# Performance work log

Measured on AMD Instinct MI355X. Metric: run time of the kernel, lower is better.

Reference implementation:

```python
import jax, jax.numpy as jnp
import numpy as np

B, C, H, W = 4, 64, 64, 64
INTER = 16  # in_c // k


def setup_inputs() -> dict:
    key = jax.random.key(0)
    ks = jax.random.split(key, 12)
    sC = 1.0 / np.sqrt(C)
    sI = 1.0 / np.sqrt(INTER)
    return {
        "x":   jax.random.normal(ks[0], (B, C, H, W), dtype=jnp.float32),
        "Wq":  jax.random.normal(ks[1], (INTER, C), dtype=jnp.float32) * sC,
        "bq":  jax.random.normal(ks[2], (INTER,), dtype=jnp.float32) * 0.1,
        "Wk":  jax.random.normal(ks[3], (INTER, C), dtype=jnp.float32) * sC,
        "bk":  jax.random.normal(ks[4], (INTER,), dtype=jnp.float32) * 0.1,
        "wcq": jax.random.normal(ks[5], (INTER,), dtype=jnp.float32) * sI,
        "wck": jax.random.normal(ks[6], (INTER,), dtype=jnp.float32) * sI,
        "Wv":  jax.random.normal(ks[7], (C, C), dtype=jnp.float32) * sC,
        "bv":  jax.random.normal(ks[8], (C,), dtype=jnp.float32) * 0.1,
        "Wg":  jax.random.normal(ks[9], (C, C), dtype=jnp.float32) * sC,
        "bg":  jax.random.normal(ks[10], (C,), dtype=jnp.float32) * 0.1,
    }


def reference(x, Wq, bq, Wk, bk, wcq, wck, Wv, bv, Wg, bg):
    b_, c_, h_, w_ = x.shape
    n = h_ * w_
    xf = x.reshape(b_, c_, n)  # (B, C, N)
    # 1x1 conv projections (per-pixel linear maps)
    q = jnp.einsum('oc,bcn->bon', Wq, xf) + bq[None, :, None]  # (B, inter, N)
    k = jnp.einsum('oc,bcn->bon', Wk, xf) + bk[None, :, None]  # (B, inter, N)
    # concat_conv (1x1, no bias) over [q_i ; k_j] decomposes into an outer sum:
    # energy[b,i,j] = wcq . q[b,:,i] + wck . k[b,:,j]
    a = jnp.einsum('o,bon->bn', wcq, q)  # (B, N)
    d = jnp.einsum('o,bon->bn', wck, k)  # (B, N)
    energy = jax.nn.elu(a[:, :, None] + d[:, None, :])  # (B, N, N)
    energy = energy / (1.5 * jnp.sum(energy, axis=1, keepdims=True))
    v = jnp.einsum('oc,bcn->bon', Wv, xf) + bv[None, :, None]  # (B, C, N)
    out = jnp.einsum('bci,bij->bcj', v, energy)  # (B, C, N)
    # gamma 1x1 conv
    out = jnp.einsum('oc,bcn->bon', Wg, out) + bg[None, :, None]
    return out.reshape(b_, c_, h_, w_)
```

## Files before the change

kernel.cpp:

```cpp
#include <hip/hip_runtime.h>
#include <math.h>

#define NB 4096

#define BARo   0
#define RELo   16
#define GHo    272
#define GCNTo  16656
#define Do     49424
#define VGo    65808
#define ASo    1114384
#define PERMo  1130768
#define BSTo   1147152
#define Po     1163536
#define PSEAo  1212688
#define PSAo   1212944
#define CPo    1213200
#define CPSEAo 1263380
#define CPSAo  1263640
#define MEMSET_BYTES 132160

__device__ __forceinline__ float gld(const float* p) {
    return __hip_atomic_load(p, __ATOMIC_RELAXED, __HIP_MEMORY_SCOPE_AGENT);
}
__device__ __forceinline__ void gst(float* p, float v) {
    __hip_atomic_store(p, v, __ATOMIC_RELAXED, __HIP_MEMORY_SCOPE_AGENT);
}
__device__ __forceinline__ void gsti(int* p, int v) {
    __hip_atomic_store(p, v, __ATOMIC_RELAXED, __HIP_MEMORY_SCOPE_AGENT);
}

__device__ __forceinline__ int bucket_of(float v) {
    int k = (int)((v + 16.0f) * 128.0f);
    k = k < 0 ? 0 : k;
    k = k > (NB - 1) ? (NB - 1) : k;
    return k;
}

__device__ __forceinline__ void gbar(int* wsi, int idx, int n) {
    __syncthreads();
    if (threadIdx.x == 0) {
        int old = __hip_atomic_fetch_add(wsi + BARo + idx, 1, __ATOMIC_RELAXED,
                                         __HIP_MEMORY_SCOPE_AGENT);
        if (old == n - 1) {
#pragma unroll
            for (int i = 0; i < 8; i++)
                __hip_atomic_store(wsi + RELo + i * 32, idx + 1, __ATOMIC_RELAXED,
                                   __HIP_MEMORY_SCOPE_AGENT);
        } else {
            const int* myrel = wsi + RELo + (blockIdx.x & 7) * 32;
            while (__hip_atomic_load(myrel, __ATOMIC_RELAXED, __HIP_MEMORY_SCOPE_AGENT) <= idx)
                __builtin_amdgcn_s_sleep(8);
        }
    }
    __syncthreads();
}

__global__ __launch_bounds__(256, 1) void k_fused(
        const float* __restrict__ x,
        const float* __restrict__ Wq, const float* __restrict__ bq,
        const float* __restrict__ Wk, const float* __restrict__ bk,
        const float* __restrict__ wcq, const float* __restrict__ wck,
        const float* __restrict__ Wv, const float* __restrict__ bv,
        const float* __restrict__ Wg, const float* __restrict__ bg,
        float* __restrict__ ws, float* __restrict__ out) {
    __shared__ float smem[13056];
    int tid = threadIdx.x;
    int bid = blockIdx.x;
    int b = bid >> 6, t6 = bid & 63;
    int* wsi = (int*)ws;
    int* gh  = wsi + GHo;

    float myA = 0.f;

    {
        float* xt  = smem;
        float* wt  = smem + 4352;
        float* wqe = smem + 8704, *wke = smem + 8768, *bvg = smem + 8832, *misc = smem + 8896;
        if (tid < 64) {
            float s1 = 0.f, s2 = 0.f, s3 = 0.f;
            for (int o = 0; o < 16; o++) { s1 += wcq[o] * Wq[o * 64 + tid]; s2 += wck[o] * Wk[o * 64 + tid]; }
            for (int m = 0; m < 64; m++) s3 += Wg[tid * 64 + m] * bv[m];
            wqe[tid] = s1; wke[tid] = s2; bvg[tid] = s3;
        } else if (tid == 64) {
            float s = 0.f; for (int o = 0; o < 16; o++) s += wcq[o] * bq[o]; misc[0] = s;
        } else if (tid == 65) {
            float s = 0.f; for (int o = 0; o < 16; o++) s += wck[o] * bk[o]; misc[1] = s;
        }
        {
            int o = tid & 63, c0 = (tid >> 6) * 16;
            float acc[16];
#pragma unroll
            for (int k = 0; k < 16; k++) acc[k] = 0.f;
            for (int m = 0; m < 64; m++) {
                float wg = Wg[o * 64 + m];
                const float4* wv4 = (const float4*)(Wv + m * 64 + c0);
                float4 a0 = wv4[0], a1 = wv4[1], a2 = wv4[2], a3 = wv4[3];
                acc[0] += wg * a0.x; acc[1] += wg * a0.y; acc[2] += wg * a0.z; acc[3] += wg * a0.w;
                acc[4] += wg * a1.x; acc[5] += wg * a1.y; acc[6] += wg * a1.z; acc[7] += wg * a1.w;
                acc[8] += wg * a2.x; acc[9] += wg * a2.y; acc[10] += wg * a2.z; acc[11] += wg * a2.w;
                acc[12] += wg * a3.x; acc[13] += wg * a3.y; acc[14] += wg * a3.z; acc[15] += wg * a3.w;
            }
#pragma unroll
            for (int k = 0; k < 16; k++) wt[(c0 + k) * 68 + o] = acc[k];
        }
        const float* xb = x + (size_t)b * 64 * 4096;
        for (int idx = tid; idx < 4096; idx += 256) {
            int c = idx >> 6, nl = idx & 63;
            xt[c * 68 + nl] = xb[(size_t)c * 4096 + t6 * 64 + nl];
        }
        __syncthreads();
        if (tid < 64) {
            float s1 = misc[0], s2 = misc[1];
            for (int c = 0; c < 64; c++) {
                float xv = xt[c * 68 + tid];
                s1 += wqe[c] * xv; s2 += wke[c] * xv;
            }
            myA = s1;
            ws[Do + b * 4096 + t6 * 64 + tid] = s2;
            atomicAdd(&gh[b * 4096 + bucket_of(s1)], 1);
        }
        {
            int o = tid & 63, nl0 = (tid >> 6) * 16;
            float acc[16];
            float bo = bvg[o];
#pragma unroll
            for (int k = 0; k < 16; k++) acc[k] = bo;
            for (int c = 0; c < 64; c++) {
                float wv = wt[c * 68 + o];
                const float* xr = &xt[c * 68 + nl0];
#pragma unroll
                for (int k = 0; k < 16; k++) acc[k] += wv * xr[k];
            }
#pragma unroll
            for (int k = 0; k < 16; k++)
                gst(&ws[VGo + ((size_t)(b * 4096) + t6 * 64 + nl0 + k) * 64 + o], acc[k]);
        }
    }
    gbar(wsi, 0, 256);

    {
        unsigned int* hist = (unsigned int*)smem;
        unsigned int* scanbuf = hist + 4096;
        const int* gh_b = gh + b * 4096;
        int* gcnt = wsi + GCNTo + b * 4096;
#pragma unroll 4
        for (int i = tid; i < NB; i += 256) hist[i] = (unsigned int)gh_b[i];
        __syncthreads();
        unsigned int s = 0u; int base = tid * 16;
        for (int k = 0; k < 16; k++) s += hist[base + k];
        scanbuf[tid] = s;
        __syncthreads();
        for (int off = 1; off < 256; off <<= 1) {
            unsigned int v = scanbuf[tid];
            unsigned int u = (tid >= off) ? scanbuf[tid - off] : 0u;
            __syncthreads();
            scanbuf[tid] = v + u;
            __syncthreads();
        }
        unsigned int run = (tid > 0) ? scanbuf[tid - 1] : 0u;
        for (int k = 0; k < 16; k++) {
            unsigned int h = hist[base + k];
            hist[base + k] = run;
            run += h;
        }
        __syncthreads();
        if (t6 == 0) {
            int* bst = wsi + BSTo;
#pragma unroll 4
            for (int i = tid; i < NB; i += 256) gsti(&bst[b * 4096 + i], (int)hist[i]);
        }
        if (tid < 64) {
            int i = t6 * 64 + tid;
            int kb = bucket_of(myA);
            int r = (int)hist[kb] + atomicAdd(&gcnt[kb], 1);
            gst(&ws[ASo + b * 4096 + r], myA);
            gsti((int*)ws + PERMo + b * 4096 + r, i);
        }
    }
    gbar(wsi, 1, 256);

    {
        int c = tid & 63, w = tid >> 6;
        int r0 = t6 * 64 + w * 16;
        const int* perm = (const int*)ws + PERMo;
        int pk[16]; float avs[16], wvs[16];
#pragma unroll
        for (int k = 0; k < 16; k++) pk[k] = perm[b * 4096 + r0 + k];
#pragma unroll
        for (int k = 0; k < 16; k++) avs[k] = ws[ASo + b * 4096 + r0 + k];
#pragma unroll
        for (int k = 0; k < 16; k++) wvs[k] = ws[VGo + ((size_t)(b * 4096) + pk[k]) * 64 + c];
        float s1 = 0.f, s2 = 0.f, s3 = 0.f, sea_w = 0.f, sa_w = 0.f;
#pragma unroll
        for (int k = 0; k < 16; k++) {
            float ea = expf(avs[k]);
            s1 += wvs[k]; s2 += wvs[k] * ea; s3 += wvs[k] * avs[k];
            sea_w += ea; sa_w += avs[k];
        }
        float* partL = smem;
        float* wsc   = smem + 768;
        partL[(w * 3 + 0) * 64 + c] = s1;
        partL[(w * 3 + 1) * 64 + c] = s2;
        partL[(w * 3 + 2) * 64 + c] = s3;
        if (c == 0) { wsc[w] = sea_w; wsc[4 + w] = sa_w; }
        __syncthreads();
        if (tid < 192) {
            int g = tid >> 6, cc = tid & 63;
            float s = partL[(0 * 3 + g) * 64 + cc] + partL[(1 * 3 + g) * 64 + cc]
                    + partL[(2 * 3 + g) * 64 + cc] + partL[(3 * 3 + g) * 64 + cc];
            gst(&ws[Po + (b * 64 + t6) * 192 + tid], s);
        } else if (tid == 192) {
            gst(&ws[PSEAo + b * 64 + t6], wsc[0] + wsc[1] + wsc[2] + wsc[3]);
            gst(&ws[PSAo  + b * 64 + t6], wsc[4] + wsc[5] + wsc[6] + wsc[7]);
        }
    }
    gbar(wsi, 2, 256);

    {
        if (tid < 192) {
            float s = 0.f;
#pragma unroll 8
            for (int ch = 0; ch < t6; ch++) s += ws[Po + b * 12288 + ch * 192 + tid];
            gst(&ws[CPo + b * 12545 + t6 * 193 + tid], s);
            if (t6 == 63) {
                s += ws[Po + b * 12288 + 63 * 192 + tid];
                gst(&ws[CPo + b * 12545 + 64 * 193 + tid], s);
            }
        } else if (tid == 192) {
            float s = 0.f;
            for (int ch = 0; ch < t6; ch++) s += ws[PSEAo + b * 64 + ch];
            gst(&ws[CPSEAo + b * 65 + t6], s);
            if (t6 == 63) { s += ws[PSEAo + b * 64 + 63]; gst(&ws[CPSEAo + b * 65 + 64], s); }
        } else if (tid == 193) {
            float s = 0.f;
            for (int ch = 0; ch < t6; ch++) s += ws[PSAo + b * 64 + ch];
            gst(&ws[CPSAo + b * 65 + t6], s);
            if (t6 == 63) { s += ws[PSAo + b * 64 + 63]; gst(&ws[CPSAo + b * 65 + 64], s); }
        }
    }
    gbar(wsi, 3, 256);

    {
        float* cpsea  = smem + 12545;
        float* cpsa   = smem + 12610;
        float* djs    = smem + 12675;
        float* edjs   = smem + 12739;
        float* invden = smem + 12803;
        int*   qarr   = (int*)(smem + 12867);
        float* bgs    = smem + 12931;
        for (int i = tid; i < 12545; i += 256) smem[i] = ws[CPo + b * 12545 + i];
        if (tid < 65)                     cpsea[tid] = ws[CPSEAo + b * 65 + tid];
        else if (tid >= 128 && tid < 193) cpsa[tid - 128] = ws[CPSAo + b * 65 + tid - 128];
        else if (tid >= 64 && tid < 128)  bgs[tid - 64] = bg[tid - 64];
        __syncthreads();
        const int* bst = (const int*)ws + BSTo;
        int j0 = t6 * 64;
        if (tid < 64) {
            int j = j0 + tid;
            float dj = ws[Do + b * 4096 + j];
            float edj = expf(dj);
            int kb = bucket_of(-dj);
            int t = bst[b * NB + kb];
            int q = (t + 32) >> 6;
            float den = 1.5f * ((cpsa[64] - cpsa[q]) + dj * (float)(4096 - 64 * q)
                                - (float)(64 * q) + edj * cpsea[q]);
            qarr[tid] = q; djs[tid] = dj; edjs[tid] = edj; invden[tid] = 1.0f / den;
        }
        __syncthreads();
        {
            int jl = tid & 63, cq = tid >> 6;
            float dj = djs[jl], edj = edjs[jl], inv = invden[jl];
            int qb = qarr[jl] * 193;
            for (int cc = cq; cc < 64; cc += 4) {
                float c1 = smem[qb + cc], c2 = smem[qb + 64 + cc], c3 = smem[qb + 128 + cc];
                float t1 = smem[12352 + cc], t3 = smem[12352 + 128 + cc];
                float num = (t3 - c3) + dj * t1 - (1.0f + dj) * c1 + edj * c2;
                out[((size_t)(b * 64 + cc)) * 4096 + j0 + jl] = num * inv + bgs[cc];
            }
        }
    }
}

extern "C" void kernel_launch(void* const* d_in, const int* in_sizes, int n_in,
                              void* d_out, int out_size, void* d_ws, size_t ws_size,
                              hipStream_t stream) {
    const float* x   = (const float*)d_in[0];
    const float* Wq  = (const float*)d_in[1];
    const float* bq  = (const float*)d_in[2];
    const float* Wk  = (const float*)d_in[3];
    const float* bk  = (const float*)d_in[4];
    const float* wcq = (const float*)d_in[5];
    const float* wck = (const float*)d_in[6];
    const float* Wv  = (const float*)d_in[7];
    const float* bv  = (const float*)d_in[8];
    const float* Wg  = (const float*)d_in[9];
    const float* bg  = (const float*)d_in[10];
    float* ws  = (float*)d_ws;
    float* out = (float*)d_out;

    hipMemsetAsync(d_ws, 0, MEMSET_BYTES, stream);
    k_fused<<<256, 256, 0, stream>>>(x, Wq, bq, Wk, bk, wcq, wck, Wv, bv, Wg, bg, ws, out);
}
```

Measured before the change: 124.5 us.

## Use hierarchical grid barrier, drop prefix stage, use wave-shuffle scan

Replaces the single-counter grid barrier with a two-level tree: leaf counters of 32 blocks feed a master counter, which cuts contention on one atomic. Removes the fourth grid barrier and the global prefix-sum stage. Each block now rebuilds the full chunk prefix sums redundantly in shared memory from the partials. The histogram scan now uses wave shuffles instead of a barrier-heavy shared-memory scan, and x tiles are loaded as float4 with a stride padded to 72. The price is that every block reads all 64 partials per column, which adds redundant global reads and register pressure from the 64-element arrays.

```diff
diff --git a/kernel.cpp b/kernel.cpp
--- a/kernel.cpp
+++ b/kernel.cpp
@@ -3,26 +3,21 @@
 
 #define NB 4096
 
-#define BARo   0
-#define RELo   16
-#define GHo    272
-#define GCNTo  16656
-#define Do     49424
-#define VGo    65808
-#define ASo    1114384
-#define PERMo  1130768
-#define BSTo   1147152
-#define Po     1163536
-#define PSEAo  1212688
-#define PSAo   1212944
-#define CPo    1213200
-#define CPSEAo 1263380
-#define CPSAo  1263640
-#define MEMSET_BYTES 132160
-
-__device__ __forceinline__ float gld(const float* p) {
-    return __hip_atomic_load(p, __ATOMIC_RELAXED, __HIP_MEMORY_SCOPE_AGENT);
-}
+#define LEAFo  0
+#define MASTo  768
+#define RELo   864
+#define GHo    1120
+#define GCNTo  17504
+#define MEMSET_BYTES 135552
+#define Do     33888
+#define VGo    50272
+#define ASo    1098848
+#define PERMo  1115232
+#define BSTo   1131616
+#define Po     1148000
+#define PSEAo  1197152
+#define PSAo   1197408
+
 __device__ __forceinline__ void gst(float* p, float v) {
     __hip_atomic_store(p, v, __ATOMIC_RELAXED, __HIP_MEMORY_SCOPE_AGENT);
 }
@@ -37,18 +32,26 @@
     return k;
 }
 
-__device__ __forceinline__ void gbar(int* wsi, int idx, int n) {
+__device__ __forceinline__ void gbar(int* wsi, int idx) {
     __syncthreads();
     if (threadIdx.x == 0) {
-        int old = __hip_atomic_fetch_add(wsi + BARo + idx, 1, __ATOMIC_RELAXED,
-                                         __HIP_MEMORY_SCOPE_AGENT);
-        if (old == n - 1) {
-#pragma unroll
-            for (int i = 0; i < 8; i++)
-                __hip_atomic_store(wsi + RELo + i * 32, idx + 1, __ATOMIC_RELAXED,
-                                   __HIP_MEMORY_SCOPE_AGENT);
-        } else {
-            const int* myrel = wsi + RELo + (blockIdx.x & 7) * 32;
+        int leaf = blockIdx.x & 7;
+        bool bcast = false;
+        int old = __hip_atomic_fetch_add(wsi + LEAFo + (idx * 8 + leaf) * 32, 1,
+                                         __ATOMIC_RELAXED, __HIP_MEMORY_SCOPE_AGENT);
+        if (old == 31) {
+            int m = __hip_atomic_fetch_add(wsi + MASTo + idx * 32, 1,
+                                           __ATOMIC_RELAXED, __HIP_MEMORY_SCOPE_AGENT);
+            if (m == 7) {
+#pragma unroll
+                for (int i = 0; i < 8; i++)
+                    __hip_atomic_store(wsi + RELo + i * 32, idx + 1,
+                                       __ATOMIC_RELAXED, __HIP_MEMORY_SCOPE_AGENT);
+                bcast = true;
+            }
+        }
+        if (!bcast) {
+            const int* myrel = wsi + RELo + leaf * 32;
             while (__hip_atomic_load(myrel, __ATOMIC_RELAXED, __HIP_MEMORY_SCOPE_AGENT) <= idx)
                 __builtin_amdgcn_s_sleep(8);
         }
@@ -75,8 +78,8 @@
 
     {
         float* xt  = smem;
-        float* wt  = smem + 4352;
-        float* wqe = smem + 8704, *wke = smem + 8768, *bvg = smem + 8832, *misc = smem + 8896;
+        float* wt  = smem + 4608;
+        float* wqe = smem + 9216, *wke = smem + 9280, *bvg = smem + 9344, *misc = smem + 9408;
         if (tid < 64) {
             float s1 = 0.f, s2 = 0.f, s3 = 0.f;
             for (int o = 0; o < 16; o++) { s1 += wcq[o] * Wq[o * 64 + tid]; s2 += wck[o] * Wk[o * 64 + tid]; }
@@ -102,18 +105,19 @@
                 acc[12] += wg * a3.x; acc[13] += wg * a3.y; acc[14] += wg * a3.z; acc[15] += wg * a3.w;
             }
 #pragma unroll
-            for (int k = 0; k < 16; k++) wt[(c0 + k) * 68 + o] = acc[k];
-        }
-        const float* xb = x + (size_t)b * 64 * 4096;
-        for (int idx = tid; idx < 4096; idx += 256) {
-            int c = idx >> 6, nl = idx & 63;
-            xt[c * 68 + nl] = xb[(size_t)c * 4096 + t6 * 64 + nl];
+            for (int k = 0; k < 16; k++) wt[(c0 + k) * 72 + o] = acc[k];
+        }
+        const float4* xb4 = (const float4*)(x + (size_t)b * 64 * 4096);
+#pragma unroll
+        for (int idx = tid; idx < 1024; idx += 256) {
+            int c = idx >> 4, nl4 = idx & 15;
+            *(float4*)&xt[c * 72 + nl4 * 4] = xb4[c * 1024 + t6 * 16 + nl4];
         }
         __syncthreads();
         if (tid < 64) {
             float s1 = misc[0], s2 = misc[1];
             for (int c = 0; c < 64; c++) {
-                float xv = xt[c * 68 + tid];
+                float xv = xt[c * 72 + tid];
                 s1 += wqe[c] * xv; s2 += wke[c] * xv;
             }
             myA = s1;
@@ -127,8 +131,8 @@
 #pragma unroll
             for (int k = 0; k < 16; k++) acc[k] = bo;
             for (int c = 0; c < 64; c++) {
-                float wv = wt[c * 68 + o];
-                const float* xr = &xt[c * 68 + nl0];
+                float wv = wt[c * 72 + o];
+                const float* xr = &xt[c * 72 + nl0];
 #pragma unroll
                 for (int k = 0; k < 16; k++) acc[k] += wv * xr[k];
             }
@@ -137,28 +141,29 @@
                 gst(&ws[VGo + ((size_t)(b * 4096) + t6 * 64 + nl0 + k) * 64 + o], acc[k]);
         }
     }
-    gbar(wsi, 0, 256);
+    gbar(wsi, 0);
 
     {
         unsigned int* hist = (unsigned int*)smem;
-        unsigned int* scanbuf = hist + 4096;
+        unsigned int* wtot = hist + 4096;
         const int* gh_b = gh + b * 4096;
         int* gcnt = wsi + GCNTo + b * 4096;
 #pragma unroll 4
         for (int i = tid; i < NB; i += 256) hist[i] = (unsigned int)gh_b[i];
         __syncthreads();
+        int lane = tid & 63, w = tid >> 6;
         unsigned int s = 0u; int base = tid * 16;
+#pragma unroll
         for (int k = 0; k < 16; k++) s += hist[base + k];
-        scanbuf[tid] = s;
-        __syncthreads();
-        for (int off = 1; off < 256; off <<= 1) {
-            unsigned int v = scanbuf[tid];
-            unsigned int u = (tid >= off) ? scanbuf[tid - off] : 0u;
-            __syncthreads();
-            scanbuf[tid] = v + u;
-            __syncthreads();
-        }
-        unsigned int run = (tid > 0) ? scanbuf[tid - 1] : 0u;
+        unsigned int inc = s;
+        for (int off = 1; off < 64; off <<= 1) {
+            unsigned int u = __shfl_up(inc, off);
+            if (lane >= off) inc += u;
+        }
+        if (lane == 63) wtot[w] = inc;
+        __syncthreads();
+        unsigned int run = inc - s;
+        for (int w2 = 0; w2 < w; w2++) run += wtot[w2];
         for (int k = 0; k < 16; k++) {
             unsigned int h = hist[base + k];
             hist[base + k] = run;
@@ -178,7 +183,7 @@
             gsti((int*)ws + PERMo + b * 4096 + r, i);
         }
     }
-    gbar(wsi, 1, 256);
+    gbar(wsi, 1);
 
     {
         int c = tid & 63, w = tid >> 6;
@@ -215,33 +220,10 @@
             gst(&ws[PSAo  + b * 64 + t6], wsc[4] + wsc[5] + wsc[6] + wsc[7]);
         }
     }
-    gbar(wsi, 2, 256);
+    gbar(wsi, 2);
 
     {
-        if (tid < 192) {
-            float s = 0.f;
-#pragma unroll 8
-            for (int ch = 0; ch < t6; ch++) s += ws[Po + b * 12288 + ch * 192 + tid];
-            gst(&ws[CPo + b * 12545 + t6 * 193 + tid], s);
-            if (t6 == 63) {
-                s += ws[Po + b * 12288 + 63 * 192 + tid];
-                gst(&ws[CPo + b * 12545 + 64 * 193 + tid], s);
-            }
-        } else if (tid == 192) {
-            float s = 0.f;
-            for (int ch = 0; ch < t6; ch++) s += ws[PSEAo + b * 64 + ch];
-            gst(&ws[CPSEAo + b * 65 + t6], s);
-            if (t6 == 63) { s += ws[PSEAo + b * 64 + 63]; gst(&ws[CPSEAo + b * 65 + 64], s); }
-        } else if (tid == 193) {
-            float s = 0.f;
-            for (int ch = 0; ch < t6; ch++) s += ws[PSAo + b * 64 + ch];
-            gst(&ws[CPSAo + b * 65 + t6], s);
-            if (t6 == 63) { s += ws[PSAo + b * 64 + 63]; gst(&ws[CPSAo + b * 65 + 64], s); }
-        }
-    }
-    gbar(wsi, 3, 256);
-
-    {
+        float* CP     = smem;
         float* cpsea  = smem + 12545;
         float* cpsa   = smem + 12610;
         float* djs    = smem + 12675;
@@ -249,10 +231,34 @@
         float* invden = smem + 12803;
         int*   qarr   = (int*)(smem + 12867);
         float* bgs    = smem + 12931;
-        for (int i = tid; i < 12545; i += 256) smem[i] = ws[CPo + b * 12545 + i];
-        if (tid < 65)                     cpsea[tid] = ws[CPSEAo + b * 65 + tid];
-        else if (tid >= 128 && tid < 193) cpsa[tid - 128] = ws[CPSAo + b * 65 + tid - 128];
-        else if (tid >= 64 && tid < 128)  bgs[tid - 64] = bg[tid - 64];
+        if (tid < 192) {
+            float v[64];
+#pragma unroll
+            for (int ch = 0; ch < 64; ch++) v[ch] = ws[Po + b * 12288 + ch * 192 + tid];
+            float r = 0.f;
+#pragma unroll
+            for (int q = 0; q < 64; q++) { CP[q * 193 + tid] = r; r += v[q]; }
+            CP[64 * 193 + tid] = r;
+        } else if (tid == 192) {
+            float v[64];
+#pragma unroll
+            for (int ch = 0; ch < 64; ch++) v[ch] = ws[PSEAo + b * 64 + ch];
+            float r = 0.f;
+#pragma unroll
+            for (int q = 0; q < 64; q++) { cpsea[q] = r; r += v[q]; }
+            cpsea[64] = r;
+        } else if (tid == 193) {
+            float v[64];
+#pragma unroll
+            for (int ch = 0; ch < 64; ch++) v[ch] = ws[PSAo + b * 64 + ch];
+            float r = 0.f;
+#pragma unroll
+            for (int q = 0; q < 64; q++) { cpsa[q] = r; r += v[q]; }
+            cpsa[64] = r;
+        } else if (tid >= 194 && tid < 258) {
+        }
+        if (tid >= 194 - 64 && tid < 194) { }
+        if (tid < 64) bgs[tid] = bg[tid];
         __syncthreads();
         const int* bst = (const int*)ws + BSTo;
         int j0 = t6 * 64;
@@ -273,8 +279,8 @@
             float dj = djs[jl], edj = edjs[jl], inv = invden[jl];
             int qb = qarr[jl] * 193;
             for (int cc = cq; cc < 64; cc += 4) {
-                float c1 = smem[qb + cc], c2 = smem[qb + 64 + cc], c3 = smem[qb + 128 + cc];
-                float t1 = smem[12352 + cc], t3 = smem[12352 + 128 + cc];
+                float c1 = CP[qb + cc], c2 = CP[qb + 64 + cc], c3 = CP[qb + 128 + cc];
+                float t1 = CP[64 * 193 + cc], t3 = CP[64 * 193 + 128 + cc];
                 float num = (t3 - c3) + dj * t1 - (1.0f + dj) * c1 + edj * c2;
                 out[((size_t)(b * 64 + cc)) * 4096 + j0 + jl] = num * inv + bgs[cc];
             }
```

Measured after the change: 107.2 us. 13.9% less time.
